# Kernel tuning notes

Hardware: AMD Instinct MI355X
Metric: run time of the kernel (lower is better)

The kernel has to match this reference:

```python
import jax, jax.numpy as jnp
import numpy as np
import math

D_MODEL = 2048
N_HEADS = 16
HEAD_DIM = D_MODEL // N_HEADS


def setup_inputs() -> dict:
    key = jax.random.key(0)
    k1, k2, k3, k4 = jax.random.split(key, 4)
    bs, seq = 2, 2048
    x = jax.random.normal(k1, (bs, seq, D_MODEL), dtype=jnp.float32)
    # torch nn.Linear weights are [out, in]; y = x @ W.T
    scale_q = 1.0 / math.sqrt(D_MODEL)
    Wq = jax.random.uniform(k2, (D_MODEL, D_MODEL), jnp.float32, -scale_q, scale_q)
    Wkv = jax.random.uniform(k3, (2 * HEAD_DIM, D_MODEL), jnp.float32, -scale_q, scale_q)
    Wo = jax.random.uniform(k4, (D_MODEL, D_MODEL), jnp.float32, -scale_q, scale_q)
    return {"x": x, "Wq": Wq, "Wkv": Wkv, "Wo": Wo}


def reference(x, Wq, Wkv, Wo):
    bs, seq, _ = x.shape
    q = x @ Wq.T                      # [b, s, d_model]
    kv = x @ Wkv.T                    # [b, s, 2*head_dim]
    k, v = jnp.split(kv, 2, axis=-1)  # each [b, s, head_dim] (single shared KV head)
    q = q.reshape(bs, seq, N_HEADS, HEAD_DIM).transpose(0, 2, 1, 3)  # [b, h, s, d]
    # MQA: broadcast shared K/V across heads via einsum (no explicit expand)
    attn = jnp.einsum("bhqd,bkd->bhqk", q, k) / math.sqrt(HEAD_DIM)  # [b, h, s, s]
    causal = jnp.tril(jnp.ones((seq, seq), dtype=bool))
    attn = jnp.where(causal[None, None], attn, jnp.float32(-1e9))
    attn = jax.nn.softmax(attn, axis=-1)
    out = jnp.einsum("bhqk,bkd->bhqd", attn, v)                      # [b, h, s, d]
    out = out.transpose(0, 2, 1, 3).reshape(bs, seq, D_MODEL)
    return out @ Wo.T
```

## Files before the change

### kernel.cpp

```cpp
#include <hip/hip_runtime.h>
#include <hip/hip_bf16.h>

typedef __attribute__((ext_vector_type(8))) short bf16x8;
typedef __attribute__((ext_vector_type(4))) float f32x4;
typedef __attribute__((ext_vector_type(16))) float f32x16;
typedef __attribute__((ext_vector_type(4))) ushort u16x4;

#define AS1 __attribute__((address_space(1)))
#define AS3 __attribute__((address_space(3)))

static __device__ __forceinline__ ushort f2b(float f) {
    union { float f; unsigned u; } v;
    v.f = f;
    unsigned r = v.u + 0x7FFF + ((v.u >> 16) & 1);
    return (ushort)(r >> 16);
}

__global__ __launch_bounds__(256) void cvt_all(const float* __restrict__ x,
                                               const float* __restrict__ Wq,
                                               const float* __restrict__ Wkv,
                                               const float* __restrict__ Wo,
                                               ushort* __restrict__ xb,
                                               ushort* __restrict__ wqkvb,
                                               ushort* __restrict__ wob)
{
    int i = blockIdx.x * blockDim.x + threadIdx.x;
    const int stride = gridDim.x * blockDim.x;
    for (; i < 4325376; i += stride) {
        const float4* src; ushort4* dst; int j;
        if (i < 2097152)      { src = (const float4*)x;   dst = (ushort4*)xb;              j = i; }
        else if (i < 3145728) { src = (const float4*)Wq;  dst = (ushort4*)wqkvb;           j = i - 2097152; }
        else if (i < 3276800) { src = (const float4*)Wkv; dst = (ushort4*)wqkvb + 1048576; j = i - 3145728; }
        else                  { src = (const float4*)Wo;  dst = (ushort4*)wob;             j = i - 3276800; }
        float4 v = src[j];
        ushort4 o; o.x = f2b(v.x); o.y = f2b(v.y); o.z = f2b(v.z); o.w = f2b(v.w);
        dst[j] = o;
    }
}

template<bool F32OUT>
__global__ __launch_bounds__(256) void gemm_bt(const ushort* __restrict__ A,
                                               const ushort* __restrict__ B,
                                               void* __restrict__ Cv,
                                               int M, int N, int K)
{
    __shared__ ushort As[2][128 * 32];
    __shared__ ushort Bs[2][128 * 32];
    const int tid  = threadIdx.x;
    const int lane = tid & 63;
    const int wid  = tid >> 6;
    const int l15  = lane & 15;
    const int lg   = lane >> 4;
    const int nwg8 = gridDim.x >> 3;
    const int kblk = blockIdx.x;
    const int swz  = (kblk & 7) * nwg8 + (kblk >> 3);
    const int nx   = N >> 7;
    const int brow = (swz / nx) * 128;
    const int bcol = (swz % nx) * 128;
    const int wr = wid >> 1, wc = wid & 1;

    f32x4 acc[4][4] = {};

    auto stage = [&](int bi, int k0) {
        const ushort* Ap = A + (size_t)brow * K + k0;
        const ushort* Bp = B + (size_t)bcol * K + k0;
#pragma unroll
        for (int j = 0; j < 2; ++j) {
            const int ci = wid * 2 + j;
            const int G  = ci * 64 + lane;
            const int r  = G >> 2, gc = G & 3;
            const int sgc = gc ^ ((r >> 1) & 3);
            __builtin_amdgcn_global_load_lds(
                (const AS1 void*)(Ap + (size_t)r * K + sgc * 8),
                (AS3 void*)(&As[bi][ci * 512]), 16, 0, 0);
            __builtin_amdgcn_global_load_lds(
                (const AS1 void*)(Bp + (size_t)r * K + sgc * 8),
                (AS3 void*)(&Bs[bi][ci * 512]), 16, 0, 0);
        }
    };

    stage(0, 0);
    __syncthreads();
    int cur = 0;

    for (int k0 = 0; k0 < K; k0 += 32) {
        if (k0 + 32 < K) stage(cur ^ 1, k0 + 32);

        bf16x8 af[4], bfr[4];
#pragma unroll
        for (int m = 0; m < 4; ++m) {
            int row = wr * 64 + m * 16 + l15;
            int slot = lg ^ ((row >> 1) & 3);
            af[m] = *(const bf16x8*)(&As[cur][row * 32 + slot * 8]);
        }
#pragma unroll
        for (int n = 0; n < 4; ++n) {
            int row = wc * 64 + n * 16 + l15;
            int slot = lg ^ ((row >> 1) & 3);
            bfr[n] = *(const bf16x8*)(&Bs[cur][row * 32 + slot * 8]);
        }
#pragma unroll
        for (int m = 0; m < 4; ++m)
#pragma unroll
            for (int n = 0; n < 4; ++n)
                acc[m][n] = __builtin_amdgcn_mfma_f32_16x16x32_bf16(af[m], bfr[n], acc[m][n], 0, 0, 0);

        __syncthreads();
        cur ^= 1;
    }

#pragma unroll
    for (int m = 0; m < 4; ++m)
#pragma unroll
        for (int n = 0; n < 4; ++n) {
            int row0 = brow + wr * 64 + m * 16 + lg * 4;
            int col  = bcol + wc * 64 + n * 16 + l15;
#pragma unroll
            for (int j = 0; j < 4; ++j) {
                float v = acc[m][n][j];
                if (F32OUT)
                    ((float*)Cv)[(size_t)(row0 + j) * N + col] = v;
                else
                    ((ushort*)Cv)[(size_t)(row0 + j) * N + col] = f2b(v);
            }
        }
}

#define QKV_PHASE(MH, NH, STG) do {                                                      \
    STG;                                                                                 \
    if (NH == 0) {                                                                       \
        _Pragma("unroll")                                                                \
        for (int m = 0; m < 4; ++m) {                                                    \
            _Pragma("unroll")                                                            \
            for (int kh = 0; kh < 2; ++kh) {                                             \
                int r  = MH * 128 + wr * 64 + m * 16 + l15;                              \
                int sl = (kh * 4 + lg) ^ (r & 7);                                        \
                af[m][kh] = *(const bf16x8*)(&Asm[cur][r * 64 + sl * 8]);                \
            }                                                                            \
        }                                                                                \
    }                                                                                    \
    _Pragma("unroll")                                                                    \
    for (int n = 0; n < 2; ++n) {                                                        \
        _Pragma("unroll")                                                                \
        for (int kh = 0; kh < 2; ++kh) {                                                 \
            int r  = NH * 128 + wc * 32 + n * 16 + l15;                                  \
            int sl = (kh * 4 + lg) ^ (r & 7);                                            \
            bf[n][kh] = *(const bf16x8*)(&Bsm[cur][r * 64 + sl * 8]);                    \
        }                                                                                \
    }                                                                                    \
    __builtin_amdgcn_s_setprio(1);                                                       \
    _Pragma("unroll")                                                                    \
    for (int m = 0; m < 4; ++m) {                                                        \
        _Pragma("unroll")                                                                \
        for (int n = 0; n < 2; ++n) {                                                    \
            acc[MH * 4 + m][NH * 2 + n] = __builtin_amdgcn_mfma_f32_16x16x32_bf16(       \
                af[m][0], bf[n][0], acc[MH * 4 + m][NH * 2 + n], 0, 0, 0);               \
            acc[MH * 4 + m][NH * 2 + n] = __builtin_amdgcn_mfma_f32_16x16x32_bf16(       \
                af[m][1], bf[n][1], acc[MH * 4 + m][NH * 2 + n], 0, 0, 0);               \
        }                                                                                \
    }                                                                                    \
    __builtin_amdgcn_s_setprio(0);                                                       \
    asm volatile("s_waitcnt lgkmcnt(0)" ::: "memory");                                   \
    asm volatile("s_waitcnt vmcnt(6)" ::: "memory");                                     \
    __builtin_amdgcn_s_barrier();                                                        \
} while (0)

__global__ __launch_bounds__(512, 2) void gemm_qkv8(const ushort* __restrict__ A,
                                                    const ushort* __restrict__ B,
                                                    ushort* __restrict__ Cq,
                                                    ushort* __restrict__ Ckv,
                                                    ushort* __restrict__ Vt)
{
    constexpr int K  = 2048;
    constexpr int NT = 32;
    __shared__ ushort Asm[2][16384];
    __shared__ ushort Bsm[2][16384];

    const int tid  = threadIdx.x;
    const int lane = tid & 63;
    const int wid  = tid >> 6;
    const int l15  = lane & 15;
    const int lg   = lane >> 4;
    const int wr   = wid >> 2;
    const int wc   = wid & 3;
    const int bid  = blockIdx.x;
    const int swz  = (bid & 7) * 18 + (bid >> 3);
    const int brow = (swz / 9) * 256;
    const int bcol = (swz % 9) * 256;

    f32x4  acc[8][4] = {};
    bf16x8 af[4][2], bf[2][2];

    auto stageH = [&](int bi, int which, int t) {
        const int k0 = t << 6;
        const ushort* src;
        ushort* dst;
        if (which == 0)      { src = A + (size_t)brow * K + k0;         dst = &Asm[bi][0];    }
        else if (which == 1) { src = A + (size_t)(brow + 128) * K + k0; dst = &Asm[bi][8192]; }
        else if (which == 2) { src = B + (size_t)bcol * K + k0;         dst = &Bsm[bi][0];    }
        else                 { src = B + (size_t)(bcol + 128) * K + k0; dst = &Bsm[bi][8192]; }
#pragma unroll
        for (int j = 0; j < 2; ++j) {
            const int t8 = j * 512 + tid;
            const int r  = t8 >> 3;
            const int s  = (t8 & 7) ^ (r & 7);
            __builtin_amdgcn_global_load_lds(
                (const AS1 void*)(src + (size_t)r * K + s * 8),
                (AS3 void*)(dst + (j * 512 + (wid << 6)) * 8), 16, 0, 0);
        }
    };

    stageH(0, 0, 0); stageH(0, 1, 0); stageH(0, 2, 0); stageH(0, 3, 0);
    stageH(1, 0, 1); stageH(1, 2, 1);
    asm volatile("s_waitcnt vmcnt(6)" ::: "memory");
    __builtin_amdgcn_s_barrier();

#pragma unroll 1
    for (int t = 0; t < NT; ++t) {
        const int cur = t & 1;
        const int nxt = cur ^ 1;
        QKV_PHASE(0, 0, { if (t + 1 < NT) stageH(nxt, 1, t + 1); });
        QKV_PHASE(0, 1, { if (t + 1 < NT) stageH(nxt, 3, t + 1); });
        QKV_PHASE(1, 0, { if (t + 2 < NT) stageH(cur, 0, t + 2); });
        QKV_PHASE(1, 1, { if (t + 2 < NT) stageH(cur, 2, t + 2); });
    }

#pragma unroll
    for (int MH = 0; MH < 2; ++MH)
#pragma unroll
    for (int m = 0; m < 4; ++m)
#pragma unroll
    for (int NH = 0; NH < 2; ++NH)
#pragma unroll
    for (int n = 0; n < 2; ++n) {
        const int row0 = brow + MH * 128 + wr * 64 + m * 16 + lg * 4;
        const int col  = bcol + NH * 128 + wc * 32 + n * 16 + l15;
        const f32x4 v4 = acc[MH * 4 + m][NH * 2 + n];
#pragma unroll
        for (int j = 0; j < 4; ++j) {
            const float v = v4[j];
            const int row = row0 + j;
            if (col < 2048) {
                Cq[(size_t)row * 2048 + col] = f2b(v);
            } else if (col < 2176) {
                Ckv[(size_t)row * 256 + (col - 2048)] = f2b(v);
            } else {
                Vt[((size_t)((row >> 11) * 128 + (col - 2176))) * 2048 + (row & 2047)] = f2b(v);
            }
        }
    }
}

__global__ __launch_bounds__(256, 2) void mqa_attn12(const ushort* __restrict__ Q,
                                                     const ushort* __restrict__ KV,
                                                     const ushort* __restrict__ Vt,
                                                     ushort* __restrict__ O)
{
    const int tid = threadIdx.x, lane = tid & 63, wid = tid >> 6;
    const int c31 = lane & 31, H = lane >> 5;
    const int bid = blockIdx.x;
    const int a  = bid & 31;
    const int hp = (bid >> 5) & 7;
    const int b  = bid >> 8;
    const int h  = hp * 2 + (wid >> 1);
    const int p  = wid & 1;

    __shared__ __align__(16) ushort SMEM[32768];

    const ushort* KVb = KV + (size_t)b * 2048 * 256;
    const ushort* Vtb = Vt + (size_t)b * 128 * 2048;
    const float C2 = 0.12751763f;
    const float mC = 32.0f * C2;

    auto stageK = [&](int buf, int par, int t) {
        ushort* dst = SMEM + (buf * 2 + par) * 4096;
        const int kvb = t * 32;
#pragma unroll
        for (int i = 0; i < 8; ++i) {
            int G = i * 64 + lane;
            int r = G >> 4, gc = G & 15;
            int sgc = gc ^ (r & 15);
            __builtin_amdgcn_global_load_lds(
                (const AS1 void*)(KVb + (size_t)(kvb + r) * 256 + sgc * 8),
                (AS3 void*)(dst + i * 512), 16, 0, 0);
        }
    };
    auto stageV = [&](int buf, int par, int t) {
        ushort* dst = SMEM + 16384 + (buf * 2 + par) * 4096;
        const int kvb = t * 32;
#pragma unroll
        for (int i = 0; i < 8; ++i) {
            int G = i * 64 + lane;
            int g = G >> 3, s = G & 7;
            int u = s ^ (g & 7);
            int r = 2 * g + (u & 1);
            int cc = u >> 1;
            __builtin_amdgcn_global_load_lds(
                (const AS1 void*)(Vtb + (size_t)r * 2048 + kvb + cc * 8),
                (AS3 void*)(dst + G * 8), 16, 0, 0);
        }
    };

#pragma unroll 1
    for (int phase = 0; phase < 2; ++phase) {
        const int tile  = phase ? (63 - a) : a;
        const int qtile = tile * 32;
        const int U = tile + 1;
        const int S = (U + 1) >> 1;
        const size_t qrow = (size_t)(b * 2048 + qtile + c31);

        bf16x8 qf[8];
#pragma unroll
        for (int dk = 0; dk < 8; ++dk)
            qf[dk] = *(const bf16x8*)(Q + qrow * 2048 + h * 128 + dk * 16 + H * 8);

        float l_run = 0.f;
        f32x16 of[4];
#pragma unroll
        for (int dt = 0; dt < 4; ++dt)
#pragma unroll
            for (int r = 0; r < 16; ++r) of[dt][r] = 0.f;

        {
            int t = p;
            if (t < U) { if (wid < 2) stageK(0, p, t); else stageV(0, p, t); }
        }
        __syncthreads();

#pragma unroll 1
        for (int s = 0; s < S; ++s) {
            if (s + 1 < S) {
                int tn = 2 * (s + 1) + p;
                if (tn < U) { if (wid < 2) stageK((s + 1) & 1, p, tn); else stageV((s + 1) & 1, p, tn); }
            }
            const int t = 2 * s + p;
            if (t < U) {
                const ushort* Kb = SMEM + ((s & 1) * 2 + p) * 4096;
                const ushort* Vb = SMEM + 16384 + ((s & 1) * 2 + p) * 4096;
                const bool maskt = (t == tile);

                f32x16 sg = {0,0,0,0,0,0,0,0,0,0,0,0,0,0,0,0};
                __builtin_amdgcn_s_setprio(1);
#pragma unroll
                for (int dk = 0; dk < 8; ++dk) {
                    bf16x8 kf = *(const bf16x8*)(Kb + c31 * 128 + ((dk * 16 + H * 8) ^ ((c31 & 15) << 3)));
                    sg = __builtin_amdgcn_mfma_f32_32x32x16_bf16(kf, qf[dk], sg, 0, 0, 0);
                }
                __builtin_amdgcn_s_setprio(0);

                float e[16];
#pragma unroll
                for (int r = 0; r < 16; ++r) {
                    float v = sg[r];
                    if (maskt) {
                        int crow = (r & 3) + 8 * (r >> 2) + 4 * H;
                        if (crow > c31) v = -1e30f;
                    }
                    e[r] = __builtin_amdgcn_exp2f(__builtin_fmaf(v, C2, -mC));
                }
                float rsum = 0.f;
#pragma unroll
                for (int r = 0; r < 16; ++r) rsum += e[r];
                rsum += __shfl_xor(rsum, 32);
                l_run += rsum;

                unsigned pk[8];
#pragma unroll
                for (int i = 0; i < 8; ++i)
                    asm("v_cvt_pk_bf16_f32 %0, %1, %2" : "=v"(pk[i]) : "v"(e[2 * i]), "v"(e[2 * i + 1]));
                asm("v_permlane32_swap_b32 %0, %1" : "+v"(pk[0]), "+v"(pk[2]));
                asm("v_permlane32_swap_b32 %0, %1" : "+v"(pk[1]), "+v"(pk[3]));
                asm("v_permlane32_swap_b32 %0, %1" : "+v"(pk[4]), "+v"(pk[6]));
                asm("v_permlane32_swap_b32 %0, %1" : "+v"(pk[5]), "+v"(pk[7]));
                union { unsigned u[4]; bf16x8 v; } P0, P1;
                P0.u[0] = pk[0]; P0.u[1] = pk[1]; P0.u[2] = pk[2]; P0.u[3] = pk[3];
                P1.u[0] = pk[4]; P1.u[1] = pk[5]; P1.u[2] = pk[6]; P1.u[3] = pk[7];

                __builtin_amdgcn_s_setprio(1);
#pragma unroll
                for (int dt = 0; dt < 4; ++dt) {
                    int g  = dt * 16 + (c31 >> 1);
                    int sw = g & 7;
                    int b0 = c31 & 1;
                    int s0 = (2 * H + b0) ^ sw;
                    int s1 = (4 + 2 * H + b0) ^ sw;
                    bf16x8 v0 = *(const bf16x8*)(Vb + (g * 8 + s0) * 8);
                    bf16x8 v1 = *(const bf16x8*)(Vb + (g * 8 + s1) * 8);
                    of[dt] = __builtin_amdgcn_mfma_f32_32x32x16_bf16(v0, P0.v, of[dt], 0, 0, 0);
                    of[dt] = __builtin_amdgcn_mfma_f32_32x32x16_bf16(v1, P1.v, of[dt], 0, 0, 0);
                }
                __builtin_amdgcn_s_setprio(0);
            }
            __syncthreads();
        }

        float* mlb = (float*)SMEM;
        if (H == 0) mlb[wid * 32 + c31] = l_run;
        __syncthreads();
        {
            float lo = mlb[(wid ^ 1) * 32 + c31];
            float inv = 1.0f / (l_run + lo);
            float* ob = (float*)(SMEM + 512) + (wid >> 1) * 4096;
            if (p == 1) {
#pragma unroll
                for (int dt = 0; dt < 4; ++dt)
#pragma unroll
                    for (int rq = 0; rq < 4; ++rq) {
                        f32x4 w;
#pragma unroll
                        for (int j = 0; j < 4; ++j) w[j] = of[dt][rq * 4 + j];
                        *(f32x4*)(ob + ((dt * 4 + rq) * 64 + lane) * 4) = w;
                    }
            }
            __syncthreads();
            if (p == 0) {
                ushort* Orow = O + qrow * 2048 + h * 128;
#pragma unroll
                for (int dt = 0; dt < 4; ++dt)
#pragma unroll
                    for (int rq = 0; rq < 4; ++rq) {
                        f32x4 r4 = *(const f32x4*)(ob + ((dt * 4 + rq) * 64 + lane) * 4);
                        u16x4 o4;
#pragma unroll
                        for (int j = 0; j < 4; ++j)
                            o4[j] = f2b((of[dt][rq * 4 + j] + r4[j]) * inv);
                        int d0 = dt * 32 + rq * 8 + 4 * H;
                        *(u16x4*)(Orow + d0) = o4;
                    }
            }
        }
        __syncthreads();
    }
}

extern "C" void kernel_launch(void* const* d_in, const int* in_sizes, int n_in,
                              void* d_out, int out_size, void* d_ws, size_t ws_size,
                              hipStream_t stream) {
    const float* x   = (const float*)d_in[0];
    const float* Wq  = (const float*)d_in[1];
    const float* Wkv = (const float*)d_in[2];
    const float* Wo  = (const float*)d_in[3];

    char* ws = (char*)d_ws;
    ushort* xb    = (ushort*)(ws);
    ushort* wqkvb = (ushort*)(ws + 16777216);
    ushort* wob   = (ushort*)(ws + 35651584);
    ushort* qb    = (ushort*)(ws + 44040192);
    ushort* kvb   = (ushort*)(ws + 60817408);
    ushort* vtb   = (ushort*)(ws + 62914560);
    ushort* aob   = xb;

    cvt_all<<<2048, 256, 0, stream>>>(x, Wq, Wkv, Wo, xb, wqkvb, wob);

    gemm_qkv8<<<144, 512, 0, stream>>>(xb, wqkvb, qb, kvb, vtb);
    mqa_attn12<<<512, 256, 0, stream>>>(qb, kvb, vtb, aob);
    gemm_bt<true><<<512, 256, 0, stream>>>(aob, wob, d_out, 4096, 2048, 2048);
}
```

Baseline: 203.5 us.

## Restructure QKV GEMM pipeline to issue stages after LDS reads with finer waits

Measured after the change: 189.9 us. 6.7% less time.

```diff
diff --git a/kernel.cpp b/kernel.cpp
--- a/kernel.cpp
+++ b/kernel.cpp
@@ -126,8 +126,9 @@
         }
 }
 
-#define QKV_PHASE(MH, NH, STG) do {                                                      \
-    STG;                                                                                 \
+#define VMW4 asm volatile("s_waitcnt vmcnt(4)" ::: "memory")
+#define VMW0 asm volatile("s_waitcnt vmcnt(0)" ::: "memory")
+#define QKV_PHASE(BUF, MH, NH, STG, DRN) do {                                            \
     if (NH == 0) {                                                                       \
         _Pragma("unroll")                                                                \
         for (int m = 0; m < 4; ++m) {                                                    \
@@ -135,7 +136,7 @@
             for (int kh = 0; kh < 2; ++kh) {                                             \
                 int r  = MH * 128 + wr * 64 + m * 16 + l15;                              \
                 int sl = (kh * 4 + lg) ^ (r & 7);                                        \
-                af[m][kh] = *(const bf16x8*)(&Asm[cur][r * 64 + sl * 8]);                \
+                af[m][kh] = *(const bf16x8*)(&Asm[BUF][r * 64 + sl * 8]);                \
             }                                                                            \
         }                                                                                \
     }                                                                                    \
@@ -145,9 +146,12 @@
         for (int kh = 0; kh < 2; ++kh) {                                                 \
             int r  = NH * 128 + wc * 32 + n * 16 + l15;                                  \
             int sl = (kh * 4 + lg) ^ (r & 7);                                            \
-            bf[n][kh] = *(const bf16x8*)(&Bsm[cur][r * 64 + sl * 8]);                    \
+            bf[n][kh] = *(const bf16x8*)(&Bsm[BUF][r * 64 + sl * 8]);                    \
         }                                                                                \
     }                                                                                    \
+    STG;                                                                                 \
+    __builtin_amdgcn_s_barrier();                                                        \
+    asm volatile("s_waitcnt lgkmcnt(0)" ::: "memory");                                   \
     __builtin_amdgcn_s_setprio(1);                                                       \
     _Pragma("unroll")                                                                    \
     for (int m = 0; m < 4; ++m) {                                                        \
@@ -160,8 +164,7 @@
         }                                                                                \
     }                                                                                    \
     __builtin_amdgcn_s_setprio(0);                                                       \
-    asm volatile("s_waitcnt lgkmcnt(0)" ::: "memory");                                   \
-    asm volatile("s_waitcnt vmcnt(6)" ::: "memory");                                     \
+    DRN;                                                                                 \
     __builtin_amdgcn_s_barrier();                                                        \
 } while (0)
 
@@ -171,8 +174,7 @@
                                                     ushort* __restrict__ Ckv,
                                                     ushort* __restrict__ Vt)
 {
-    constexpr int K  = 2048;
-    constexpr int NT = 32;
+    constexpr int K = 2048;
     __shared__ ushort Asm[2][16384];
     __shared__ ushort Bsm[2][16384];
 
@@ -210,20 +212,31 @@
         }
     };
 
-    stageH(0, 0, 0); stageH(0, 1, 0); stageH(0, 2, 0); stageH(0, 3, 0);
+    stageH(0, 0, 0); stageH(0, 2, 0); stageH(0, 1, 0); stageH(0, 3, 0);
     stageH(1, 0, 1); stageH(1, 2, 1);
-    asm volatile("s_waitcnt vmcnt(6)" ::: "memory");
+    VMW4;
     __builtin_amdgcn_s_barrier();
 
 #pragma unroll 1
-    for (int t = 0; t < NT; ++t) {
-        const int cur = t & 1;
-        const int nxt = cur ^ 1;
-        QKV_PHASE(0, 0, { if (t + 1 < NT) stageH(nxt, 1, t + 1); });
-        QKV_PHASE(0, 1, { if (t + 1 < NT) stageH(nxt, 3, t + 1); });
-        QKV_PHASE(1, 0, { if (t + 2 < NT) stageH(cur, 0, t + 2); });
-        QKV_PHASE(1, 1, { if (t + 2 < NT) stageH(cur, 2, t + 2); });
+    for (int i = 0; i < 15; ++i) {
+        const int t1 = 2 * i + 1;
+        QKV_PHASE(0, 0, 0, { stageH(1, 1, t1); stageH(1, 3, t1); }, ((void)0));
+        QKV_PHASE(0, 0, 1, { stageH(0, 0, t1 + 1); },               ((void)0));
+        QKV_PHASE(0, 1, 0, { ((void)0); },                          ((void)0));
+        QKV_PHASE(0, 1, 1, { stageH(0, 2, t1 + 1); },               VMW4);
+        QKV_PHASE(1, 0, 0, { stageH(0, 1, t1 + 1); stageH(0, 3, t1 + 1); }, ((void)0));
+        QKV_PHASE(1, 0, 1, { stageH(1, 0, t1 + 2); },               ((void)0));
+        QKV_PHASE(1, 1, 0, { ((void)0); },                          ((void)0));
+        QKV_PHASE(1, 1, 1, { stageH(1, 2, t1 + 2); },               VMW4);
     }
+    QKV_PHASE(0, 0, 0, { stageH(1, 1, 31); stageH(1, 3, 31); }, ((void)0));
+    QKV_PHASE(0, 0, 1, { ((void)0); }, ((void)0));
+    QKV_PHASE(0, 1, 0, { ((void)0); }, ((void)0));
+    QKV_PHASE(0, 1, 1, { ((void)0); }, VMW0);
+    QKV_PHASE(1, 0, 0, { ((void)0); }, ((void)0));
+    QKV_PHASE(1, 0, 1, { ((void)0); }, ((void)0));
+    QKV_PHASE(1, 1, 0, { ((void)0); }, ((void)0));
+    QKV_PHASE(1, 1, 1, { ((void)0); }, ((void)0));
 
 #pragma unroll
     for (int MH = 0; MH < 2; ++MH)
```
